# Performance work log

Hardware: AMD Instinct MI355X
Metric: run time of the kernel (lower is better)

## Reference

```python
import jax, jax.numpy as jnp
import numpy as np

HEAD_SIZE = 64


def setup_inputs() -> dict:
    key = jax.random.key(0)
    kx, kq, kk, kv = jax.random.split(key, 4)
    B, L, D = 4, 4096, 1024
    scale = 1.0 / np.sqrt(D)
    x = jax.random.normal(kx, (B, L, D), dtype=jnp.float32)
    Wq = jax.random.normal(kq, (D, HEAD_SIZE), dtype=jnp.float32) * scale
    Wk = jax.random.normal(kk, (D, HEAD_SIZE), dtype=jnp.float32) * scale
    Wv = jax.random.normal(kv, (D, HEAD_SIZE), dtype=jnp.float32) * scale
    return {"x": x, "Wq": Wq, "Wk": Wk, "Wv": Wv}


def reference(x, Wq, Wk, Wv):
    B, L, D = x.shape
    H = Wq.shape[1]
    q = jnp.einsum('bld,dh->blh', x, Wq)  # [B,L,H]
    k = jnp.einsum('bld,dh->blh', x, Wk)
    v = jnp.einsum('bld,dh->blh', x, Wv)
    # full L x L score matrix, as in the original module
    scores = jnp.einsum('bqh,bkh->bqk', q, k) / jnp.sqrt(jnp.float32(H))
    causal = jnp.tril(jnp.ones((L, L), dtype=bool))
    scores = jnp.where(causal, scores, -jnp.inf)
    attn = jax.nn.softmax(scores, axis=-1)
    z = jnp.einsum('bqk,bkh->bqh', attn, v)  # [B,L,H]
    return z
```

## Files before the change

### kernel.cpp

```cpp
#include <hip/hip_runtime.h>
#include <stdint.h>

#define L_SEQ 4096
#define D_MODEL 1024
#define HEAD 64
#define KCH 512
#define MAXCH 8
#define NQT 32

typedef unsigned short u16;
typedef _Float16 f16;
typedef __attribute__((ext_vector_type(8))) f16 f16x8;
typedef __attribute__((ext_vector_type(2))) __fp16 fp16x2;
typedef __attribute__((ext_vector_type(4))) float f32x4;

static __device__ __forceinline__ u16 f16bits(float f) {
    union { f16 h; u16 u; } c; c.h = (f16)f; return c.u;
}
static __device__ __forceinline__ uint32_t pk16(float a, float b) {
    union { fp16x2 h; uint32_t u; } c;
    c.h = __builtin_amdgcn_cvt_pkrtz(a, b);
    return c.u;
}
static __device__ __forceinline__ f16x8 ld8h(const u16* p) { return *(const f16x8*)p; }

static __device__ __forceinline__ f32x4 mfma16h(f16x8 a, f16x8 b, f32x4 c) {
    return __builtin_amdgcn_mfma_f32_16x16x32_f16(a, b, c, 0, 0, 0);
}

static __device__ __forceinline__ void gload16(const u16* g, u16* l) {
    __builtin_amdgcn_global_load_lds(
        (const __attribute__((address_space(1))) void*)g,
        (__attribute__((address_space(3))) void*)l, 16, 0, 0);
}

static __device__ __forceinline__ int Sq(int qt) {
    int f = qt >> 2, r = qt & 3;
    return (f + 1) * (2 * f + r);
}

__global__ __launch_bounds__(256) void conv_w(
    const float* __restrict__ Wq, const float* __restrict__ Wk,
    const float* __restrict__ Wv, u16* __restrict__ Wt)
{
    __shared__ u16 tile[64][72];
    const float* W = (blockIdx.y == 0) ? Wq : (blockIdx.y == 1) ? Wk : Wv;
    const float sc = (blockIdx.y == 0) ? 0.18033688f : 1.0f;
    u16* dst = Wt + blockIdx.y * (HEAD * D_MODEL);
    const int k0 = blockIdx.x * 64, t = threadIdx.x;
    #pragma unroll
    for (int i = 0; i < 16; i++) {
        int idx = i * 256 + t;
        int kk = idx >> 6, h = idx & 63;
        tile[h][kk] = f16bits(W[(size_t)(k0 + kk) * HEAD + h] * sc);
    }
    __syncthreads();
    #pragma unroll
    for (int i = 0; i < 16; i++) {
        int idx = i * 256 + t;
        int h = idx >> 6, kk = idx & 63;
        dst[(size_t)h * D_MODEL + k0 + kk] = tile[h][kk];
    }
}

__global__ __launch_bounds__(256, 4) void qkv_proj(
    const float* __restrict__ x, const u16* __restrict__ Wt,
    u16* __restrict__ qb, u16* __restrict__ kb, u16* __restrict__ vTb)
{
    __shared__ __align__(16) u16 Wl[2 * 192 * 32];
    __shared__ __align__(16) u16 Xl[2 * 32 * 36];
#define WLX(dh,r,c) Wl[((dh)*192 + (r))*32 + (c)]
#define XLX(kh,r,c) Xl[((kh)*32  + (r))*36 + (c)]
#define CT(r,c)     Wl[(r)*200 + (c)]

    const int t = threadIdx.x;
    const int wv = t >> 6, lane = t & 63;
    const int ln16 = lane & 15, quad = lane >> 4;
    const int w3 = wv * 3;
    const int m0 = blockIdx.x * 32;

    f32x4 acc[2][3] = {};
    float4 xv0, xv1;

    auto issueW = [&](int s) {
        const int k0 = s * 64;
        #pragma unroll
        for (int k2 = 0; k2 < 6; k2++) {
            int c = wv * 6 + k2;
            int dh = c & 1, g = c >> 1;
            const u16* gp = Wt + (size_t)(g * 16 + (lane >> 2)) * D_MODEL
                               + k0 + dh * 32 + (lane & 3) * 8;
            gload16(gp, &WLX(dh, g * 16 + (lane >> 2), (lane & 3) * 8));
        }
    };
    auto loadx = [&](int s) {
        const int k0 = s * 64;
        int r0 = t >> 4, cs0 = (t & 15) * 4;
        xv0 = *(const float4*)&x[(size_t)(m0 + r0) * D_MODEL + k0 + cs0];
        int idx = 256 + t, r1 = idx >> 4, cs1 = (idx & 15) * 4;
        xv1 = *(const float4*)&x[(size_t)(m0 + r1) * D_MODEL + k0 + cs1];
    };
    auto packx = [&]() {
        int r0 = t >> 4, cs0 = (t & 15) * 4;
        uint2 p0; p0.x = pk16(xv0.x, xv0.y); p0.y = pk16(xv0.z, xv0.w);
        *(uint2*)&XLX(cs0 >> 5, r0, cs0 & 31) = p0;
        int idx = 256 + t, r1 = idx >> 4, cs1 = (idx & 15) * 4;
        uint2 p1; p1.x = pk16(xv1.x, xv1.y); p1.y = pk16(xv1.z, xv1.w);
        *(uint2*)&XLX(cs1 >> 5, r1, cs1 & 31) = p1;
    };

    loadx(0); issueW(0); packx();
    for (int s = 0; s < 16; s++) {
        __syncthreads();
        f16x8 xb[2][2], af[2][3];
        #pragma unroll
        for (int c = 0; c < 2; c++) {
            xb[c][0] = ld8h(&XLX(c, ln16, quad * 8));
            xb[c][1] = ld8h(&XLX(c, 16 + ln16, quad * 8));
            #pragma unroll
            for (int j = 0; j < 3; j++)
                af[c][j] = ld8h(&WLX(c, (w3 + j) * 16 + ln16, quad * 8));
        }
        #pragma unroll
        for (int c = 0; c < 2; c++)
            #pragma unroll
            for (int j = 0; j < 3; j++) {
                acc[0][j] = mfma16h(af[c][j], xb[c][0], acc[0][j]);
                acc[1][j] = mfma16h(af[c][j], xb[c][1], acc[1][j]);
            }
        if (s + 1 < 16) loadx(s + 1);
        __syncthreads();
        if (s + 1 < 16) { issueW(s + 1); packx(); }
    }

    __syncthreads();
    #pragma unroll
    for (int mt = 0; mt < 2; mt++) {
        #pragma unroll
        for (int j = 0; j < 3; j++) {
            int g0 = (w3 + j) * 16 + quad * 4;
            uint2 pk;
            pk.x = pk16(acc[mt][j][0], acc[mt][j][1]);
            pk.y = pk16(acc[mt][j][2], acc[mt][j][3]);
            *(uint2*)&CT(mt * 16 + ln16, g0) = pk;
        }
    }
    __syncthreads();
    {
        int m = t >> 3, hg = (t & 7) * 8;
        *(f16x8*)&qb[(size_t)(m0 + m) * HEAD + hg] = *(f16x8*)&CT(m, hg);
        *(f16x8*)&kb[(size_t)(m0 + m) * HEAD + hg] = *(f16x8*)&CT(m, 64 + hg);
        int h = t >> 2, mg = (t & 3) * 8;
        f16x8 vvv;
        #pragma unroll
        for (int jj = 0; jj < 8; jj++)
            ((u16*)&vvv)[jj] = CT(mg + jj, 128 + h);
        int bbt = m0 >> 12, l0 = m0 & 4095;
        *(f16x8*)&vTb[(size_t)(bbt * HEAD + h) * L_SEQ + l0 + mg] = vvv;
    }
#undef WLX
#undef XLX
#undef CT
}

__global__ __launch_bounds__(256, 4) void attn_chunk(
    const u16* __restrict__ qb, const u16* __restrict__ kb,
    const u16* __restrict__ vT, float* __restrict__ Opart, float* __restrict__ lpart)
{
    const int qt = blockIdx.x, ch = blockIdx.y, b = blockIdx.z;
    if (ch * KCH > qt * 128 + 127) return;

    __shared__ __align__(16) u16 Kls[2 * 64 * 32];
    __shared__ __align__(16) u16 Vls[2 * 64 * 32];
    __shared__ __align__(16) u16 Pls[4 * 32 * 72];
#define KBX(dh,r,c) Kls[((dh)*64 + (r))*32 + (c)]
#define VBX(kh,r,c) Vls[((kh)*64 + (r))*32 + (c)]
#define PX(r,c)     Pls[((wv)*32 + (r))*72 + (c)]

    const int t = threadIdx.x, wv = t >> 6, lane = t & 63;
    const int ln16 = lane & 15, quad = lane >> 4;
    const int qmin = qt * 128 + wv * 32;

    f16x8 qf[2][2];
    #pragma unroll
    for (int qn = 0; qn < 2; qn++) {
        const u16* qrp = qb + (size_t)(b * L_SEQ + qmin + qn * 16 + ln16) * HEAD + quad * 8;
        qf[qn][0] = ld8h(qrp); qf[qn][1] = ld8h(qrp + 32);
    }

    const u16* kbb = kb + (size_t)b * L_SEQ * HEAD;
    const u16* vbb = vT + (size_t)b * HEAD * L_SEQ;

    f32x4 o[2][4] = {};
    float lsum[2] = {0.f, 0.f};

    const int kv_lo = ch * KCH;
    const int kv_hi = min(kv_lo + KCH, qt * 128 + 128);
    const int nst = (kv_hi - kv_lo) >> 6;

    auto issue_stage = [&](int kv0) {
        #pragma unroll
        for (int k2 = 0; k2 < 4; k2++) {
            int c = wv * 4 + k2;
            if (c < 8) {
                int dh = c & 1, g = c >> 1;
                const u16* gp = kbb + (size_t)(kv0 + g * 16 + (lane >> 2)) * HEAD
                                    + dh * 32 + (lane & 3) * 8;
                gload16(gp, &KBX(dh, g * 16 + (lane >> 2), (lane & 3) * 8));
            } else {
                int c2 = c - 8, kh = c2 & 1, g = c2 >> 1;
                const u16* gp = vbb + (size_t)(g * 16 + (lane >> 2)) * L_SEQ
                                    + kv0 + kh * 32 + (lane & 3) * 8;
                gload16(gp, &VBX(kh, g * 16 + (lane >> 2), (lane & 3) * 8));
            }
        }
    };

    for (int s = 0; s < nst; s++) {
        const int kv0 = kv_lo + s * 64;
        issue_stage(kv0);
        __syncthreads();

        #pragma unroll
        for (int g = 0; g < 4; g++) {
            f16x8 ka0 = ld8h(&KBX(0, g * 16 + ln16, quad * 8));
            f16x8 ka1 = ld8h(&KBX(1, g * 16 + ln16, quad * 8));
            #pragma unroll
            for (int qn = 0; qn < 2; qn++) {
                f32x4 s2 = {};
                s2 = mfma16h(ka0, qf[qn][0], s2);
                s2 = mfma16h(ka1, qf[qn][1], s2);
                float p0, p1, p2, p3;
                if (kv0 + g * 16 + 15 <= qmin + qn * 16) {
                    p0 = __builtin_amdgcn_exp2f(s2[0]);
                    p1 = __builtin_amdgcn_exp2f(s2[1]);
                    p2 = __builtin_amdgcn_exp2f(s2[2]);
                    p3 = __builtin_amdgcn_exp2f(s2[3]);
                } else {
                    int q = qmin + qn * 16 + ln16;
                    int kv = kv0 + g * 16 + quad * 4;
                    p0 = (kv     <= q) ? __builtin_amdgcn_exp2f(s2[0]) : 0.f;
                    p1 = (kv + 1 <= q) ? __builtin_amdgcn_exp2f(s2[1]) : 0.f;
                    p2 = (kv + 2 <= q) ? __builtin_amdgcn_exp2f(s2[2]) : 0.f;
                    p3 = (kv + 3 <= q) ? __builtin_amdgcn_exp2f(s2[3]) : 0.f;
                }
                lsum[qn] += (p0 + p1) + (p2 + p3);
                uint2 pk; pk.x = pk16(p0, p1); pk.y = pk16(p2, p3);
                *(uint2*)&PX(qn * 16 + ln16, g * 16 + quad * 4) = pk;
            }
        }
        f16x8 pf[2][2];
        #pragma unroll
        for (int qn = 0; qn < 2; qn++) {
            pf[qn][0] = ld8h(&PX(qn * 16 + ln16, quad * 8));
            pf[qn][1] = ld8h(&PX(qn * 16 + ln16, 32 + quad * 8));
        }
        #pragma unroll
        for (int hg = 0; hg < 4; hg++) {
            f16x8 va0 = ld8h(&VBX(0, hg * 16 + ln16, quad * 8));
            f16x8 va1 = ld8h(&VBX(1, hg * 16 + ln16, quad * 8));
            #pragma unroll
            for (int qn = 0; qn < 2; qn++) {
                o[qn][hg] = mfma16h(va0, pf[qn][0], o[qn][hg]);
                o[qn][hg] = mfma16h(va1, pf[qn][1], o[qn][hg]);
            }
        }
        __syncthreads();
    }

    #pragma unroll
    for (int qn = 0; qn < 2; qn++) {
        lsum[qn] += __shfl_xor(lsum[qn], 16);
        lsum[qn] += __shfl_xor(lsum[qn], 32);
    }

    const size_t base = (size_t)(b * 144 + Sq(qt) + ch);
    #pragma unroll
    for (int qn = 0; qn < 2; qn++) {
        int q_local = wv * 32 + qn * 16 + ln16;
        #pragma unroll
        for (int hg = 0; hg < 4; hg++)
            *(f32x4*)&Opart[base * 8192 + (size_t)q_local * 64 + hg * 16 + quad * 4] = o[qn][hg];
        if (quad == 0)
            lpart[base * 128 + q_local] = lsum[qn];
    }
#undef KBX
#undef VBX
#undef PX
}

__global__ __launch_bounds__(256) void merge_chunks(
    const float* __restrict__ Opart, const float* __restrict__ lpart,
    float* __restrict__ out)
{
    const int qt = blockIdx.x, qseg = blockIdx.y, b = blockIdx.z;
    const int nch = (qt + 4) >> 2;
    const int t = threadIdx.x;
    const size_t obase = (size_t)(b * 144 + Sq(qt)) * 8192;
    const size_t lbase = (size_t)(b * 144 + Sq(qt)) * 128;
    #pragma unroll
    for (int i = 0; i < 2; i++) {
        int idx = i * 256 + t;
        int q = qseg * 32 + (idx >> 4), hg = (idx & 15) * 4;
        float L = 0.f, ax = 0.f, ay = 0.f, az = 0.f, aw = 0.f;
        #pragma unroll
        for (int c = 0; c < MAXCH; c++) {
            if (c < nch) {
                L += lpart[lbase + c * 128 + q];
                const float4 v = *(const float4*)&Opart[obase + (size_t)c * 8192 + q * 64 + hg];
                ax += v.x; ay += v.y; az += v.z; aw += v.w;
            }
        }
        float inv = 1.f / L;
        float4 r; r.x = ax * inv; r.y = ay * inv; r.z = az * inv; r.w = aw * inv;
        *(float4*)&out[((size_t)(b * L_SEQ + qt * 128 + q)) * HEAD + hg] = r;
    }
}

extern "C" void kernel_launch(void* const* d_in, const int* in_sizes, int n_in,
                              void* d_out, int out_size, void* d_ws, size_t ws_size,
                              hipStream_t stream) {
    const float* x  = (const float*)d_in[0];
    const float* Wq = (const float*)d_in[1];
    const float* Wk = (const float*)d_in[2];
    const float* Wv = (const float*)d_in[3];
    float* out = (float*)d_out;

    u16* ws16 = (u16*)d_ws;
    u16* Wt  = ws16;
    u16* qb  = Wt + 3 * HEAD * D_MODEL;
    u16* kb  = qb + 16384 * HEAD;
    u16* vTb = kb + 16384 * HEAD;
    float* Opart = (float*)(vTb + 16384 * HEAD);
    float* lpart = Opart + (size_t)4 * 144 * 8192;

    conv_w      <<<dim3(16, 3), 256, 0, stream>>>(Wq, Wk, Wv, Wt);
    qkv_proj    <<<dim3(512), 256, 0, stream>>>(x, Wt, qb, kb, vTb);
    attn_chunk  <<<dim3(NQT, MAXCH, 4), 256, 0, stream>>>(qb, kb, vTb, Opart, lpart);
    merge_chunks<<<dim3(NQT, 4, 4), 256, 0, stream>>>(Opart, lpart, out);
}
```

Baseline: 152.7 us.

## Double-buffer K/V tiles, store fp16 partials, write single-chunk tiles directly

Attention staging now uses two LDS buffers for K/V, so the next tile's global loads are issued before computing on the current one, and one barrier per iteration is dropped. Partial O accumulators are stored as fp16 instead of fp32, halving partial-output traffic. Query tiles with only one KV chunk normalize and write the final output directly. The merge kernel then handles only the remaining tiles with one block per tile. This adds LDS use (occupancy bound lowered to 3) and fp16 rounding of unnormalized partial sums.

```diff
diff --git a/kernel.cpp b/kernel.cpp
--- a/kernel.cpp
+++ b/kernel.cpp
@@ -163,23 +163,25 @@
 #undef CT
 }
 
-__global__ __launch_bounds__(256, 4) void attn_chunk(
+__global__ __launch_bounds__(256, 3) void attn_chunk(
     const u16* __restrict__ qb, const u16* __restrict__ kb,
-    const u16* __restrict__ vT, float* __restrict__ Opart, float* __restrict__ lpart)
+    const u16* __restrict__ vT, u16* __restrict__ OpartH,
+    float* __restrict__ lpart, float* __restrict__ out)
 {
     const int qt = blockIdx.x, ch = blockIdx.y, b = blockIdx.z;
     if (ch * KCH > qt * 128 + 127) return;
 
-    __shared__ __align__(16) u16 Kls[2 * 64 * 32];
-    __shared__ __align__(16) u16 Vls[2 * 64 * 32];
+    __shared__ __align__(16) u16 Kls[2 * 2 * 64 * 32];
+    __shared__ __align__(16) u16 Vls[2 * 2 * 64 * 32];
     __shared__ __align__(16) u16 Pls[4 * 32 * 72];
-#define KBX(dh,r,c) Kls[((dh)*64 + (r))*32 + (c)]
-#define VBX(kh,r,c) Vls[((kh)*64 + (r))*32 + (c)]
-#define PX(r,c)     Pls[((wv)*32 + (r))*72 + (c)]
+#define KBX(bb,dh,r,c) Kls[(((bb)*2 + (dh))*64 + (r))*32 + (c)]
+#define VBX(bb,kh,r,c) Vls[(((bb)*2 + (kh))*64 + (r))*32 + (c)]
+#define PX(r,c)        Pls[((wv)*32 + (r))*72 + (c)]
 
     const int t = threadIdx.x, wv = t >> 6, lane = t & 63;
     const int ln16 = lane & 15, quad = lane >> 4;
     const int qmin = qt * 128 + wv * 32;
+    const int nch = (qt + 4) >> 2;
 
     f16x8 qf[2][2];
     #pragma unroll
@@ -198,7 +200,7 @@
     const int kv_hi = min(kv_lo + KCH, qt * 128 + 128);
     const int nst = (kv_hi - kv_lo) >> 6;
 
-    auto issue_stage = [&](int kv0) {
+    auto issue_stage = [&](int kv0, int bb) {
         #pragma unroll
         for (int k2 = 0; k2 < 4; k2++) {
             int c = wv * 4 + k2;
@@ -206,25 +208,27 @@
                 int dh = c & 1, g = c >> 1;
                 const u16* gp = kbb + (size_t)(kv0 + g * 16 + (lane >> 2)) * HEAD
                                     + dh * 32 + (lane & 3) * 8;
-                gload16(gp, &KBX(dh, g * 16 + (lane >> 2), (lane & 3) * 8));
+                gload16(gp, &KBX(bb, dh, g * 16 + (lane >> 2), (lane & 3) * 8));
             } else {
                 int c2 = c - 8, kh = c2 & 1, g = c2 >> 1;
                 const u16* gp = vbb + (size_t)(g * 16 + (lane >> 2)) * L_SEQ
                                     + kv0 + kh * 32 + (lane & 3) * 8;
-                gload16(gp, &VBX(kh, g * 16 + (lane >> 2), (lane & 3) * 8));
+                gload16(gp, &VBX(bb, kh, g * 16 + (lane >> 2), (lane & 3) * 8));
             }
         }
     };
 
+    issue_stage(kv_lo, 0);
+    int buf = 0;
     for (int s = 0; s < nst; s++) {
         const int kv0 = kv_lo + s * 64;
-        issue_stage(kv0);
         __syncthreads();
+        if (s + 1 < nst) issue_stage(kv0 + 64, buf ^ 1);
 
         #pragma unroll
         for (int g = 0; g < 4; g++) {
-            f16x8 ka0 = ld8h(&KBX(0, g * 16 + ln16, quad * 8));
-            f16x8 ka1 = ld8h(&KBX(1, g * 16 + ln16, quad * 8));
+            f16x8 ka0 = ld8h(&KBX(buf, 0, g * 16 + ln16, quad * 8));
+            f16x8 ka1 = ld8h(&KBX(buf, 1, g * 16 + ln16, quad * 8));
             #pragma unroll
             for (int qn = 0; qn < 2; qn++) {
                 f32x4 s2 = {};
@@ -257,15 +261,15 @@
         }
         #pragma unroll
         for (int hg = 0; hg < 4; hg++) {
-            f16x8 va0 = ld8h(&VBX(0, hg * 16 + ln16, quad * 8));
-            f16x8 va1 = ld8h(&VBX(1, hg * 16 + ln16, quad * 8));
+            f16x8 va0 = ld8h(&VBX(buf, 0, hg * 16 + ln16, quad * 8));
+            f16x8 va1 = ld8h(&VBX(buf, 1, hg * 16 + ln16, quad * 8));
             #pragma unroll
             for (int qn = 0; qn < 2; qn++) {
                 o[qn][hg] = mfma16h(va0, pf[qn][0], o[qn][hg]);
                 o[qn][hg] = mfma16h(va1, pf[qn][1], o[qn][hg]);
             }
         }
-        __syncthreads();
+        buf ^= 1;
     }
 
     #pragma unroll
@@ -274,13 +278,32 @@
         lsum[qn] += __shfl_xor(lsum[qn], 32);
     }
 
+    if (nch == 1) {
+        #pragma unroll
+        for (int qn = 0; qn < 2; qn++) {
+            float inv = 1.f / lsum[qn];
+            int qg = qmin + qn * 16 + ln16;
+            #pragma unroll
+            for (int hg = 0; hg < 4; hg++) {
+                f32x4 r = o[qn][hg];
+                float4 w; w.x = r[0] * inv; w.y = r[1] * inv; w.z = r[2] * inv; w.w = r[3] * inv;
+                *(float4*)&out[((size_t)(b * L_SEQ + qg)) * HEAD + hg * 16 + quad * 4] = w;
+            }
+        }
+        return;
+    }
+
     const size_t base = (size_t)(b * 144 + Sq(qt) + ch);
     #pragma unroll
     for (int qn = 0; qn < 2; qn++) {
         int q_local = wv * 32 + qn * 16 + ln16;
         #pragma unroll
-        for (int hg = 0; hg < 4; hg++)
-            *(f32x4*)&Opart[base * 8192 + (size_t)q_local * 64 + hg * 16 + quad * 4] = o[qn][hg];
+        for (int hg = 0; hg < 4; hg++) {
+            uint2 pk;
+            pk.x = pk16(o[qn][hg][0], o[qn][hg][1]);
+            pk.y = pk16(o[qn][hg][2], o[qn][hg][3]);
+            *(uint2*)&OpartH[base * 8192 + (size_t)q_local * 64 + hg * 16 + quad * 4] = pk;
+        }
         if (quad == 0)
             lpart[base * 128 + q_local] = lsum[qn];
     }
@@ -290,30 +313,28 @@
 }
 
 __global__ __launch_bounds__(256) void merge_chunks(
-    const float* __restrict__ Opart, const float* __restrict__ lpart,
+    const u16* __restrict__ OpartH, const float* __restrict__ lpart,
     float* __restrict__ out)
 {
-    const int qt = blockIdx.x, qseg = blockIdx.y, b = blockIdx.z;
+    const int qt = blockIdx.x + 4, b = blockIdx.y;
     const int nch = (qt + 4) >> 2;
     const int t = threadIdx.x;
-    const size_t obase = (size_t)(b * 144 + Sq(qt)) * 8192;
-    const size_t lbase = (size_t)(b * 144 + Sq(qt)) * 128;
-    #pragma unroll
-    for (int i = 0; i < 2; i++) {
+    const int slot0 = b * 144 + Sq(qt);
+    #pragma unroll
+    for (int i = 0; i < 8; i++) {
         int idx = i * 256 + t;
-        int q = qseg * 32 + (idx >> 4), hg = (idx & 15) * 4;
-        float L = 0.f, ax = 0.f, ay = 0.f, az = 0.f, aw = 0.f;
-        #pragma unroll
-        for (int c = 0; c < MAXCH; c++) {
-            if (c < nch) {
-                L += lpart[lbase + c * 128 + q];
-                const float4 v = *(const float4*)&Opart[obase + (size_t)c * 8192 + q * 64 + hg];
-                ax += v.x; ay += v.y; az += v.z; aw += v.w;
-            }
+        int q = idx >> 4, hgp = idx & 15;
+        float L = 0.f, a0 = 0.f, a1 = 0.f, a2 = 0.f, a3 = 0.f;
+        for (int c = 0; c < nch; c++) {
+            L += lpart[(size_t)(slot0 + c) * 128 + q];
+            union { uint2 u; f16 h[4]; } v;
+            v.u = *(const uint2*)&OpartH[(size_t)(slot0 + c) * 8192 + q * 64 + hgp * 4];
+            a0 += (float)v.h[0]; a1 += (float)v.h[1];
+            a2 += (float)v.h[2]; a3 += (float)v.h[3];
         }
         float inv = 1.f / L;
-        float4 r; r.x = ax * inv; r.y = ay * inv; r.z = az * inv; r.w = aw * inv;
-        *(float4*)&out[((size_t)(b * L_SEQ + qt * 128 + q)) * HEAD + hg] = r;
+        float4 r; r.x = a0 * inv; r.y = a1 * inv; r.z = a2 * inv; r.w = a3 * inv;
+        *(float4*)&out[((size_t)(b * L_SEQ + qt * 128 + q)) * HEAD + hgp * 4] = r;
     }
 }
 
@@ -331,11 +352,11 @@
     u16* qb  = Wt + 3 * HEAD * D_MODEL;
     u16* kb  = qb + 16384 * HEAD;
     u16* vTb = kb + 16384 * HEAD;
-    float* Opart = (float*)(vTb + 16384 * HEAD);
-    float* lpart = Opart + (size_t)4 * 144 * 8192;
+    u16* OpartH = vTb + 16384 * HEAD;
+    float* lpart = (float*)(OpartH + (size_t)4 * 144 * 8192);
 
     conv_w      <<<dim3(16, 3), 256, 0, stream>>>(Wq, Wk, Wv, Wt);
     qkv_proj    <<<dim3(512), 256, 0, stream>>>(x, Wt, qb, kb, vTb);
-    attn_chunk  <<<dim3(NQT, MAXCH, 4), 256, 0, stream>>>(qb, kb, vTb, Opart, lpart);
-    merge_chunks<<<dim3(NQT, 4, 4), 256, 0, stream>>>(Opart, lpart, out);
-}
+    attn_chunk  <<<dim3(NQT, MAXCH, 4), 256, 0, stream>>>(qb, kb, vTb, OpartH, lpart, out);
+    merge_chunks<<<dim3(28, 4), 256, 0, stream>>>(OpartH, lpart, out);
+}
```

After: 166.5 us. 9.1% more time.
